# Performance work log

Measured on AMD Instinct MI355X. Metric: run time of the kernel, lower is better.

Reference implementation:

```python
import jax, jax.numpy as jnp
import numpy as np

NV, NF, DIM = 6144, 12288, 256


def _linear(x, W, b):
    # torch nn.Linear: x @ W.T + b, W has shape (out, in)
    return x @ W.T + b


def _agg(X, A, Wf, bf, Wg, bg):
    # AGG: out_fc = Linear(A @ X); out_gagg = Linear(A @ out_fc)  (eval mode: dropout is identity)
    out_fc = _linear(A @ X, Wf, bf)
    out_g = _linear(A @ out_fc, Wg, bg)
    return jax.nn.relu(out_fc + out_g)


def setup_inputs() -> dict:
    key = jax.random.key(0)
    ks = jax.random.split(key, 18)
    primal = jax.random.normal(ks[0], (NV, DIM), jnp.float32)
    # degree-normalized adjacency (docstring): scale uniform entries by 1/N for stable row sums
    A_primal = jax.random.uniform(ks[1], (NV, NV), jnp.float32) * (1.0 / NV)
    A_dual = jax.random.uniform(ks[2], (NF, NF), jnp.float32) * (1.0 / NF)
    A = jax.random.uniform(ks[3], (NV, NF), jnp.float32) * (1.0 / NF)
    faces = jax.random.randint(ks[4], (NF, 3), 0, NV)

    w = lambda k, shp: jax.random.normal(k, shp, jnp.float32) * 0.05
    return {
        "primal": primal, "A_primal": A_primal, "A_dual": A_dual, "A": A, "faces": faces,
        # 3 primal AGG layers (fc + gagg), stacked on leading axis
        "pW": w(ks[5], (3, DIM, DIM)), "pb": w(ks[6], (3, DIM)),
        "pgW": w(ks[7], (3, DIM, DIM)), "pgb": w(ks[8], (3, DIM)),
        # 3 dual AGG layers
        "dW": w(ks[9], (3, DIM, DIM)), "db": w(ks[10], (3, DIM)),
        "dgW": w(ks[11], (3, DIM, DIM)), "dgb": w(ks[12], (3, DIM)),
        # PDF linears: (dim, 2*dim)
        "Wp": w(ks[13], (DIM, 2 * DIM)), "bp": w(ks[14], (DIM,)),
        "Wd": w(ks[15], (DIM, 2 * DIM)), "bd": w(ks[16], (DIM,)),
    }


def reference(primal, A_primal, A_dual, A, faces, pW, pb, pgW, pgb, dW, db, dgW, dgb, Wp, bp, Wd, bd):
    x_p = primal
    x_d = (1.0 / 3.0) * (A.T @ primal)  # primal_dual
    primal_outs, dual_outs = [], []
    for i in range(3):
        primal_outs.append(x_p)
        x_p = _agg(x_p, A_primal, pW[i], pb[i], pgW[i], pgb[i]) + x_p
    for i in range(3):
        dual_outs.append(x_d)
        x_d = _agg(x_d, A_dual, dW[i], db[i], dgW[i], dgb[i]) + x_d
    # PDF: DAP gather-reduce  (N_f, 3, dim) -> (N_f, dim)
    f = jnp.mean(jnp.abs(x_p[faces] - x_d[:, None, :]), axis=1)
    out_dual = jax.nn.relu(_linear(jnp.concatenate([x_d, f], axis=1), Wd, bd))
    mapped = A @ f  # dual_primal
    out_primal = jax.nn.relu(_linear(jnp.concatenate([x_p, mapped], axis=1), Wp, bp))
    return (out_primal + x_p, out_dual + x_d, *primal_outs, *dual_outs)
```

## Files before the change

### kernel.cpp

```cpp
#include <hip/hip_runtime.h>


typedef short short8 __attribute__((ext_vector_type(8)));
typedef float floatx4 __attribute__((ext_vector_type(4)));
typedef unsigned short u16;

#define DIMN 256
#define GBM 128
#define GBN 256
#define GBK 64

static const int kNV = 6144;
static const int kNF = 12288;
static const int SLAB = 768;

__device__ __forceinline__ float bf2f(u16 u) {
  union { unsigned int i; float f; } x; x.i = ((unsigned int)u) << 16; return x.f;
}
__device__ __forceinline__ u16 f2bf(float f) {
  union { float f; unsigned int i; } x; x.f = f;
  unsigned int r = x.i + 0x7fffu + ((x.i >> 16) & 1u);
  return (u16)(r >> 16);
}
__device__ __forceinline__ void gld_lds16(const void* g, void* l) {
  __builtin_amdgcn_global_load_lds((__attribute__((address_space(1))) void*)(g),
                                   (__attribute__((address_space(3))) void*)(l),
                                   16, 0, 0);
}

__global__ __launch_bounds__(512, 1)
void gemm_bf16_k(const void* __restrict__ A0, int A0is32,
                 const void* __restrict__ A1, int A1is32, int K1,
                 int lda0, int lda1,
                 const void* __restrict__ Bt, int Btis32, int ldb,
                 float* __restrict__ P, int M, int kchunk)
{
  __shared__ __align__(16) u16 As[2][GBM * GBK];
  __shared__ __align__(16) u16 Bs[2][GBN * GBK];

  const int m0 = blockIdx.x * GBM;
  const int kb = blockIdx.z * kchunk;
  const int nkt = kchunk / GBK;

  const int tid = threadIdx.x;
  const int wid = tid >> 6;
  const int lane = tid & 63;
  const int wr = wid >> 2;
  const int wc = wid & 3;
  const int srow = lane >> 3;
  const int skk = (lane & 7) << 3;

  floatx4 acc[4][4];
  floatx4 zz = {0.f, 0.f, 0.f, 0.f};
#pragma unroll
  for (int i = 0; i < 4; ++i)
#pragma unroll
    for (int j = 0; j < 4; ++j) acc[i][j] = zz;

  auto stage = [&](int buf, int k0) {
    const void* base; int lda, is32, kl;
    if (k0 < K1) { base = A0; lda = lda0; is32 = A0is32; kl = k0; }
    else         { base = A1; lda = lda1; is32 = A1is32; kl = k0 - K1; }
    if (is32) {
      const float* F = (const float*)base;
#pragma unroll
      for (int j = 0; j < 2; ++j) {
        int c = (wid << 1) + j;
        const float* src = F + (size_t)(m0 + (c << 3) + srow) * lda + kl + skk;
        floatx4 f0 = *(const floatx4*)src;
        floatx4 f1 = *(const floatx4*)(src + 4);
        short8 v;
#pragma unroll
        for (int e = 0; e < 4; ++e) { v[e] = (short)f2bf(f0[e]); v[4 + e] = (short)f2bf(f1[e]); }
        *(short8*)&As[buf][(c << 9) + (lane << 3)] = v;
      }
    } else {
      const u16* U = (const u16*)base;
#pragma unroll
      for (int j = 0; j < 2; ++j) {
        int c = (wid << 1) + j;
        gld_lds16(U + (size_t)(m0 + (c << 3) + srow) * lda + kl + skk,
                  (void*)&As[buf][c << 9]);
      }
    }
    if (Btis32) {
      const float* F = (const float*)Bt;
#pragma unroll
      for (int j = 0; j < 4; ++j) {
        int c = (wid << 2) + j;
        const float* src = F + (size_t)((c << 3) + srow) * ldb + k0 + skk;
        floatx4 f0 = *(const floatx4*)src;
        floatx4 f1 = *(const floatx4*)(src + 4);
        short8 v;
#pragma unroll
        for (int e = 0; e < 4; ++e) { v[e] = (short)f2bf(f0[e]); v[4 + e] = (short)f2bf(f1[e]); }
        *(short8*)&Bs[buf][(c << 9) + (lane << 3)] = v;
      }
    } else {
      const u16* U = (const u16*)Bt;
#pragma unroll
      for (int j = 0; j < 4; ++j) {
        int c = (wid << 2) + j;
        gld_lds16(U + (size_t)((c << 3) + srow) * ldb + k0 + skk,
                  (void*)&Bs[buf][c << 9]);
      }
    }
  };

  int cur = 0;
  stage(0, kb);
  for (int kt = 0; kt < nkt; ++kt) {
    __syncthreads();
    if (kt + 1 < nkt) stage(cur ^ 1, kb + (kt + 1) * GBK);
#pragma unroll
    for (int ks = 0; ks < 2; ++ks) {
      short8 a[4], b[4];
      const int ko = (ks << 5) + ((lane >> 4) << 3);
#pragma unroll
      for (int mi = 0; mi < 4; ++mi)
        a[mi] = *(const short8*)&As[cur][((wr << 6) + (mi << 4) + (lane & 15)) * GBK + ko];
#pragma unroll
      for (int ni = 0; ni < 4; ++ni)
        b[ni] = *(const short8*)&Bs[cur][((wc << 6) + (ni << 4) + (lane & 15)) * GBK + ko];
#pragma unroll
      for (int mi = 0; mi < 4; ++mi)
#pragma unroll
        for (int ni = 0; ni < 4; ++ni)
          acc[mi][ni] = __builtin_amdgcn_mfma_f32_16x16x32_bf16(a[mi], b[ni], acc[mi][ni], 0, 0, 0);
    }
    cur ^= 1;
  }

  float* Pz = P + (size_t)blockIdx.z * (size_t)M * DIMN;
#pragma unroll
  for (int mi = 0; mi < 4; ++mi) {
#pragma unroll
    for (int ni = 0; ni < 4; ++ni) {
      const int mb = m0 + (wr << 6) + (mi << 4) + ((lane >> 4) << 2);
      const int n = (wc << 6) + (ni << 4) + (lane & 15);
#pragma unroll
      for (int r = 0; r < 4; ++r)
        Pz[(size_t)(mb + r) * DIMN + n] = acc[mi][ni][r];
    }
  }
}

__global__ __launch_bounds__(256)
void finalize_k(const float* __restrict__ P, int S, int Mrows, float scale,
                const float* __restrict__ bias, const u16* __restrict__ addmat,
                int do_relu, const float* __restrict__ resid,
                float* __restrict__ out, u16* __restrict__ out16)
{
  const size_t MN = (size_t)Mrows * DIMN;
  const size_t i4 = (((size_t)blockIdx.x * blockDim.x) + threadIdx.x) * 4;
  if (i4 >= MN) return;
  floatx4 v = {0.f, 0.f, 0.f, 0.f};
  for (int s = 0; s < S; ++s) v += *(const floatx4*)(P + (size_t)s * MN + i4);
  const int n = (int)(i4 & 255);
  floatx4 bf = {0.f,0.f,0.f,0.f}, af = {0.f,0.f,0.f,0.f}, rf = {0.f,0.f,0.f,0.f};
  if (bias) bf = *(const floatx4*)(bias + n);
  if (addmat) {
#pragma unroll
    for (int j = 0; j < 4; ++j) af[j] = bf2f(addmat[i4 + j]);
  }
  if (resid) rf = *(const floatx4*)(resid + i4);
  floatx4 o;
#pragma unroll
  for (int j = 0; j < 4; ++j) {
    float t = v[j] * scale + bf[j] + af[j];
    if (do_relu) t = fmaxf(t, 0.f);
    o[j] = t + rf[j];
  }
  if (out) *(floatx4*)(out + i4) = o;
  if (out16) {
    unsigned long long q = 0;
#pragma unroll
    for (int j = 0; j < 4; ++j) q |= ((unsigned long long)f2bf(o[j])) << (16 * j);
    *(unsigned long long*)(out16 + i4) = q;
  }
}

__global__ __launch_bounds__(256)
void transpose_k(const void* __restrict__ in, int is32, int ldin,
                 u16* __restrict__ out, int ldout)
{
  __shared__ __align__(16) u16 t[64][64];
  const int c0 = blockIdx.x << 6;
  const int r0 = blockIdx.y << 6;
  const int tid = threadIdx.x;
  const int lr = tid >> 3;
  const int lc = (tid & 7) << 3;
#pragma unroll
  for (int h = 0; h < 2; ++h) {
    const int r = lr + (h << 5);
    short8 v;
    if (is32) {
      const float* F = (const float*)in;
      const float* src = F + (size_t)(r0 + r) * ldin + (c0 + lc);
      floatx4 f0 = *(const floatx4*)src;
      floatx4 f1 = *(const floatx4*)(src + 4);
#pragma unroll
      for (int e = 0; e < 4; ++e) { v[e] = (short)f2bf(f0[e]); v[4 + e] = (short)f2bf(f1[e]); }
    } else {
      v = *(const short8*)((const u16*)in + (size_t)(r0 + r) * ldin + (c0 + lc));
    }
    *(short8*)&t[r][lc ^ ((r >> 3) << 3)] = v;
  }
  __syncthreads();
#pragma unroll
  for (int h = 0; h < 2; ++h) {
    const int oc = lr + (h << 5);
    short8 v;
#pragma unroll
    for (int e = 0; e < 8; ++e)
      v[e] = (short)t[lc + e][oc ^ ((lc >> 3) << 3)];
    *(short8*)&out[(size_t)(c0 + oc) * ldout + (r0 + lc)] = v;
  }
}

__global__ __launch_bounds__(256)
void cvt8_k(const float* __restrict__ in, u16* __restrict__ out, size_t n)
{
  const size_t i = (((size_t)blockIdx.x << 8) + threadIdx.x) << 3;
  if (i >= n) return;
  floatx4 f0 = *(const floatx4*)(in + i);
  floatx4 f1 = *(const floatx4*)(in + i + 4);
  short8 v;
#pragma unroll
  for (int e = 0; e < 4; ++e) { v[e] = (short)f2bf(f0[e]); v[4 + e] = (short)f2bf(f1[e]); }
  *(short8*)(out + i) = v;
}

__global__ __launch_bounds__(256)
void face_gather_k(const float* __restrict__ xp, const float* __restrict__ xd,
                   const int* __restrict__ faces, u16* __restrict__ f)
{
  const int fi = blockIdx.x;
  const int j = threadIdx.x;
  const int a = faces[fi * 3 + 0];
  const int b = faces[fi * 3 + 1];
  const int c = faces[fi * 3 + 2];
  const float xv = xd[(size_t)fi * DIMN + j];
  const float s = fabsf(xp[(size_t)a * DIMN + j] - xv)
                + fabsf(xp[(size_t)b * DIMN + j] - xv)
                + fabsf(xp[(size_t)c * DIMN + j] - xv);
  f[(size_t)fi * DIMN + j] = f2bf(s * (1.0f / 3.0f));
}

extern "C" void kernel_launch(void* const* d_in, const int* in_sizes, int n_in,
                              void* d_out, int out_size, void* d_ws, size_t ws_size,
                              hipStream_t stream)
{
  (void)in_sizes; (void)n_in; (void)out_size;
  const float* primal   = (const float*)d_in[0];
  const float* A_primal = (const float*)d_in[1];
  const float* A_dual   = (const float*)d_in[2];
  const float* A        = (const float*)d_in[3];
  const int* faces      = (const int*)d_in[4];
  const float* pW  = (const float*)d_in[5];
  const float* pb  = (const float*)d_in[6];
  const float* pgW = (const float*)d_in[7];
  const float* pgb = (const float*)d_in[8];
  const float* dW  = (const float*)d_in[9];
  const float* db  = (const float*)d_in[10];
  const float* dgW = (const float*)d_in[11];
  const float* dgb = (const float*)d_in[12];
  const float* Wp  = (const float*)d_in[13];
  const float* bp  = (const float*)d_in[14];
  const float* Wd  = (const float*)d_in[15];
  const float* bd  = (const float*)d_in[16];

  char* wsp = (char*)d_ws;
  auto alloc = [&](size_t bytes) -> void* {
    void* p = (void*)wsp;
    wsp += (bytes + 255) & ~(size_t)255;
    return p;
  };
  const size_t NVD = (size_t)kNV * DIMN, NFD = (size_t)kNF * DIMN;
  u16* XT    = (u16*)alloc(NFD * 2);
  u16* TB    = (u16*)alloc((size_t)SLAB * kNV * 2);
  u16* t1    = (u16*)alloc(NFD * 2);
  u16* fc    = (u16*)alloc(NFD * 2);
  float* P   = (float*)alloc((size_t)8 * NFD * 4);
  const size_t bigElems = (size_t)kNF * kNF + (size_t)kNF * kNV +
                          (size_t)kNV * kNF + (size_t)kNV * kNV + 1048576;
  const size_t need = (size_t)(wsp - (char*)d_ws) + bigElems * 2 + 4096;
  const bool big = ws_size >= need;
  u16 *Ad16 = nullptr, *At16 = nullptr, *A16 = nullptr, *Ap16 = nullptr, *W16 = nullptr;
  if (big) {
    Ad16 = (u16*)alloc((size_t)kNF * kNF * 2);
    At16 = (u16*)alloc((size_t)kNF * kNV * 2);
    A16  = (u16*)alloc((size_t)kNV * kNF * 2);
    Ap16 = (u16*)alloc((size_t)kNV * kNV * 2);
    W16  = (u16*)alloc((size_t)1048576 * 2);
  }

  float* out0  = (float*)d_out;
  float* out1  = out0 + NVD;
  float* pouts = out1 + NFD;
  float* douts = pouts + 3 * NVD;

  auto gemm = [&](const void* A0p, int a0is32, int lda0,
                  const void* A1p, int a1is32, int lda1, int K1,
                  const void* Btp, int btis32, int ldb, int M, int K, int S) {
    gemm_bf16_k<<<dim3(M / GBM, 1, S), dim3(512), 0, stream>>>(
        A0p, a0is32, A1p, a1is32, K1, lda0, lda1, Btp, btis32, ldb, P, M, K / S);
  };
  auto fin = [&](int M, int S, float scale, const float* bias, const u16* add,
                 int relu, const float* resid, float* out, u16* out16) {
    finalize_k<<<dim3((unsigned)((size_t)M * DIMN / 1024)), dim3(256), 0, stream>>>(
        P, S, M, scale, bias, add, relu, resid, out, out16);
  };
  auto tranp = [&](const void* in, int is32, int ldin, u16* out, int ldout,
                   int R, int C) {
    transpose_k<<<dim3(C / 64, R / 64), dim3(256), 0, stream>>>(
        in, is32, ldin, out, ldout);
  };
  auto cvt = [&](const float* in, u16* out, size_t n) {
    cvt8_k<<<dim3((unsigned)(n / 2048)), dim3(256), 0, stream>>>(in, out, n);
  };

  const void *AdP, *ApP, *AP, *pWP, *pgWP, *dWP, *dgWP, *WpP, *WdP;
  int cf;
  if (big) {
    cvt(A_dual, Ad16, (size_t)kNF * kNF);
    cvt(A_primal, Ap16, (size_t)kNV * kNV);
    cvt(A, A16, (size_t)kNV * kNF);
    tranp(A, 1, kNF, At16, kNV, kNV, kNF);
    cvt(pW,  W16 + 0,      196608);
    cvt(pgW, W16 + 196608, 196608);
    cvt(dW,  W16 + 393216, 196608);
    cvt(dgW, W16 + 589824, 196608);
    cvt(Wp,  W16 + 786432, 131072);
    cvt(Wd,  W16 + 917504, 131072);
    AdP = Ad16; ApP = Ap16; AP = A16; cf = 0;
    pWP = W16; pgWP = W16 + 196608; dWP = W16 + 393216; dgWP = W16 + 589824;
    WpP = W16 + 786432; WdP = W16 + 917504;
  } else {
    AdP = A_dual; ApP = A_primal; AP = A; cf = 1;
    pWP = pW; pgWP = pgW; dWP = dW; dgWP = dgW; WpP = Wp; WdP = Wd;
  }
  const size_t W3 = 65536;

  tranp(primal, 1, DIMN, XT, kNV, kNV, DIMN);
  hipMemcpyAsync(pouts, primal, NVD * 4, hipMemcpyDeviceToDevice, stream);

  if (big) {
    gemm(At16, 0, kNV, nullptr, 0, 0, kNV, XT, 0, kNV, kNF, kNV, 8);
    fin(kNF, 8, 1.0f / 3.0f, nullptr, nullptr, 0, nullptr, douts, nullptr);
  } else {
    for (int s = 0; s < kNF / SLAB; ++s) {
      const int m0 = s * SLAB;
      tranp(A + m0, 1, kNF, TB, kNV, kNV, SLAB);
      gemm(TB, 0, kNV, nullptr, 0, 0, kNV, XT, 0, kNV, SLAB, kNV, 16);
      fin(SLAB, 16, 1.0f / 3.0f, nullptr, nullptr, 0, nullptr,
          douts + (size_t)m0 * DIMN, nullptr);
    }
  }

  const float* xpc = primal;
  for (int i = 0; i < 3; ++i) {
    gemm(ApP, cf, kNV, nullptr, 0, 0, kNV, XT, 0, kNV, kNV, kNV, 16);
    fin(kNV, 16, 1.f, nullptr, nullptr, 0, nullptr, nullptr, t1);
    gemm(t1, 0, 256, nullptr, 0, 0, 256, (const u16*)pWP + i * W3, cf, 256,
         kNV, 256, 4);
    fin(kNV, 4, 1.f, pb + i * 256, nullptr, 0, nullptr, nullptr, fc);
    tranp(fc, 0, DIMN, TB, kNV, kNV, DIMN);
    gemm(ApP, cf, kNV, nullptr, 0, 0, kNV, TB, 0, kNV, kNV, kNV, 16);
    fin(kNV, 16, 1.f, nullptr, nullptr, 0, nullptr, nullptr, t1);
    gemm(t1, 0, 256, nullptr, 0, 0, 256, (const u16*)pgWP + i * W3, cf, 256,
         kNV, 256, 4);
    float* nxt = (i < 2) ? (pouts + (size_t)(i + 1) * NVD) : out0;
    fin(kNV, 4, 1.f, pgb + i * 256, fc, 1, xpc, nxt, nullptr);
    xpc = nxt;
    if (i < 2) tranp(xpc, 1, DIMN, XT, kNV, kNV, DIMN);
  }

  const float* xdc = douts;
  tranp(xdc, 1, DIMN, XT, kNF, kNF, DIMN);
  for (int i = 0; i < 3; ++i) {
    gemm(AdP, cf, kNF, nullptr, 0, 0, kNF, XT, 0, kNF, kNF, kNF, 8);
    fin(kNF, 8, 1.f, nullptr, nullptr, 0, nullptr, nullptr, t1);
    gemm(t1, 0, 256, nullptr, 0, 0, 256, (const u16*)dWP + i * W3, cf, 256,
         kNF, 256, 4);
    fin(kNF, 4, 1.f, db + i * 256, nullptr, 0, nullptr, nullptr, fc);
    tranp(fc, 0, DIMN, TB, kNF, kNF, DIMN);
    gemm(AdP, cf, kNF, nullptr, 0, 0, kNF, TB, 0, kNF, kNF, kNF, 8);
    fin(kNF, 8, 1.f, nullptr, nullptr, 0, nullptr, nullptr, t1);
    gemm(t1, 0, 256, nullptr, 0, 0, 256, (const u16*)dgWP + i * W3, cf, 256,
         kNF, 256, 4);
    float* nxt = (i < 2) ? (douts + (size_t)(i + 1) * NFD) : out1;
    fin(kNF, 4, 1.f, dgb + i * 256, fc, 1, xdc, nxt, nullptr);
    xdc = nxt;
    if (i < 2) tranp(xdc, 1, DIMN, XT, kNF, kNF, DIMN);
  }

  face_gather_k<<<dim3(kNF), dim3(256), 0, stream>>>(xpc, xdc, faces, t1);
  tranp(t1, 0, DIMN, TB, kNF, kNF, DIMN);
  gemm(xdc, 1, 256, t1, 0, 256, 256, WdP, cf, 512, kNF, 512, 8);
  fin(kNF, 8, 1.f, bd, nullptr, 1, xdc, out1, nullptr);
  gemm(AP, cf, kNF, nullptr, 0, 0, kNF, TB, 0, kNF, kNV, kNF, 16);
  fin(kNV, 16, 1.f, nullptr, nullptr, 0, nullptr, nullptr, fc);
  gemm(xpc, 1, 256, fc, 0, 256, 256, WpP, cf, 512, kNV, 512, 8);
  fin(kNV, 8, 1.f, bp, nullptr, 1, xpc, out0, nullptr);
}
```

Before: 2.162 ms.

## Fuse linear epilogues into GEMM, store split-K partials as bf16, drop conversions

The small 256-wide linear GEMMs now run without split-K and apply bias, add, relu and residual directly in the GEMM epilogue. This removes their separate finalize launches and the fp32 partial round trip. The big adjacency GEMMs write split-K partials in bf16 instead of fp32, halving partial-buffer traffic at some cost in precision. The weight and A bf16 conversion passes are also dropped: weights and A are read as fp32 and converted inside the GEMM, trading the upfront cvt work for in-kernel conversion and a single-block-per-row grid on the linear GEMMs.

```diff
diff --git a/kernel.cpp b/kernel.cpp
--- a/kernel.cpp
+++ b/kernel.cpp
@@ -3,6 +3,7 @@
 
 typedef short short8 __attribute__((ext_vector_type(8)));
 typedef float floatx4 __attribute__((ext_vector_type(4)));
+typedef unsigned short ushort4v __attribute__((ext_vector_type(4)));
 typedef unsigned short u16;
 
 #define DIMN 256
@@ -33,7 +34,11 @@
                  const void* __restrict__ A1, int A1is32, int K1,
                  int lda0, int lda1,
                  const void* __restrict__ Bt, int Btis32, int ldb,
-                 float* __restrict__ P, int M, int kchunk)
+                 void* __restrict__ P, int M, int kchunk, int pbf16,
+                 int fused, const float* __restrict__ bias,
+                 const u16* __restrict__ addmat, int do_relu,
+                 const float* __restrict__ resid,
+                 float* __restrict__ outf, u16* __restrict__ out16)
 {
   __shared__ __align__(16) u16 As[2][GBM * GBK];
   __shared__ __align__(16) u16 Bs[2][GBN * GBK];
@@ -131,22 +136,57 @@
     cur ^= 1;
   }
 
-  float* Pz = P + (size_t)blockIdx.z * (size_t)M * DIMN;
-#pragma unroll
-  for (int mi = 0; mi < 4; ++mi) {
-#pragma unroll
-    for (int ni = 0; ni < 4; ++ni) {
-      const int mb = m0 + (wr << 6) + (mi << 4) + ((lane >> 4) << 2);
-      const int n = (wc << 6) + (ni << 4) + (lane & 15);
-#pragma unroll
-      for (int r = 0; r < 4; ++r)
-        Pz[(size_t)(mb + r) * DIMN + n] = acc[mi][ni][r];
+  if (fused) {
+#pragma unroll
+    for (int mi = 0; mi < 4; ++mi) {
+#pragma unroll
+      for (int ni = 0; ni < 4; ++ni) {
+        const int mb = m0 + (wr << 6) + (mi << 4) + ((lane >> 4) << 2);
+        const int n = (wc << 6) + (ni << 4) + (lane & 15);
+        const float bv = bias ? bias[n] : 0.f;
+#pragma unroll
+        for (int r = 0; r < 4; ++r) {
+          const size_t idx = (size_t)(mb + r) * DIMN + n;
+          float t = acc[mi][ni][r] + bv;
+          if (addmat) t += bf2f(addmat[idx]);
+          if (do_relu) t = fmaxf(t, 0.f);
+          if (resid) t += resid[idx];
+          if (outf) outf[idx] = t;
+          if (out16) out16[idx] = f2bf(t);
+        }
+      }
+    }
+  } else if (pbf16) {
+    u16* Pz = (u16*)P + (size_t)blockIdx.z * (size_t)M * DIMN;
+#pragma unroll
+    for (int mi = 0; mi < 4; ++mi) {
+#pragma unroll
+      for (int ni = 0; ni < 4; ++ni) {
+        const int mb = m0 + (wr << 6) + (mi << 4) + ((lane >> 4) << 2);
+        const int n = (wc << 6) + (ni << 4) + (lane & 15);
+#pragma unroll
+        for (int r = 0; r < 4; ++r)
+          Pz[(size_t)(mb + r) * DIMN + n] = f2bf(acc[mi][ni][r]);
+      }
+    }
+  } else {
+    float* Pz = (float*)P + (size_t)blockIdx.z * (size_t)M * DIMN;
+#pragma unroll
+    for (int mi = 0; mi < 4; ++mi) {
+#pragma unroll
+      for (int ni = 0; ni < 4; ++ni) {
+        const int mb = m0 + (wr << 6) + (mi << 4) + ((lane >> 4) << 2);
+        const int n = (wc << 6) + (ni << 4) + (lane & 15);
+#pragma unroll
+        for (int r = 0; r < 4; ++r)
+          Pz[(size_t)(mb + r) * DIMN + n] = acc[mi][ni][r];
+      }
     }
   }
 }
 
 __global__ __launch_bounds__(256)
-void finalize_k(const float* __restrict__ P, int S, int Mrows, float scale,
+void finalize_k(const void* __restrict__ P, int pbf16, int S, int Mrows, float scale,
                 const float* __restrict__ bias, const u16* __restrict__ addmat,
                 int do_relu, const float* __restrict__ resid,
                 float* __restrict__ out, u16* __restrict__ out16)
@@ -155,7 +195,17 @@
   const size_t i4 = (((size_t)blockIdx.x * blockDim.x) + threadIdx.x) * 4;
   if (i4 >= MN) return;
   floatx4 v = {0.f, 0.f, 0.f, 0.f};
-  for (int s = 0; s < S; ++s) v += *(const floatx4*)(P + (size_t)s * MN + i4);
+  if (pbf16) {
+    const u16* Pu = (const u16*)P;
+    for (int s = 0; s < S; ++s) {
+      ushort4v p4 = *(const ushort4v*)(Pu + (size_t)s * MN + i4);
+#pragma unroll
+      for (int j = 0; j < 4; ++j) v[j] += bf2f(p4[j]);
+    }
+  } else {
+    const float* Pf = (const float*)P;
+    for (int s = 0; s < S; ++s) v += *(const floatx4*)(Pf + (size_t)s * MN + i4);
+  }
   const int n = (int)(i4 & 255);
   floatx4 bf = {0.f,0.f,0.f,0.f}, af = {0.f,0.f,0.f,0.f}, rf = {0.f,0.f,0.f,0.f};
   if (bias) bf = *(const floatx4*)(bias + n);
@@ -281,18 +331,15 @@
   u16* TB    = (u16*)alloc((size_t)SLAB * kNV * 2);
   u16* t1    = (u16*)alloc(NFD * 2);
   u16* fc    = (u16*)alloc(NFD * 2);
-  float* P   = (float*)alloc((size_t)8 * NFD * 4);
-  const size_t bigElems = (size_t)kNF * kNF + (size_t)kNF * kNV +
-                          (size_t)kNV * kNF + (size_t)kNV * kNV + 1048576;
+  void* P    = alloc((size_t)8 * NFD * 4);
+  const size_t bigElems = (size_t)kNF * kNF + (size_t)kNF * kNV + (size_t)kNV * kNV;
   const size_t need = (size_t)(wsp - (char*)d_ws) + bigElems * 2 + 4096;
   const bool big = ws_size >= need;
-  u16 *Ad16 = nullptr, *At16 = nullptr, *A16 = nullptr, *Ap16 = nullptr, *W16 = nullptr;
+  u16 *Ad16 = nullptr, *At16 = nullptr, *Ap16 = nullptr;
   if (big) {
     Ad16 = (u16*)alloc((size_t)kNF * kNF * 2);
     At16 = (u16*)alloc((size_t)kNF * kNV * 2);
-    A16  = (u16*)alloc((size_t)kNV * kNF * 2);
     Ap16 = (u16*)alloc((size_t)kNV * kNV * 2);
-    W16  = (u16*)alloc((size_t)1048576 * 2);
   }
 
   float* out0  = (float*)d_out;
@@ -300,16 +347,24 @@
   float* pouts = out1 + NFD;
   float* douts = pouts + 3 * NVD;
 
-  auto gemm = [&](const void* A0p, int a0is32, int lda0,
-                  const void* A1p, int a1is32, int lda1, int K1,
-                  const void* Btp, int btis32, int ldb, int M, int K, int S) {
+  auto gemmP = [&](const void* A0p, int a0is32, int lda0,
+                   const void* Btp, int ldb, int M, int K, int S) {
     gemm_bf16_k<<<dim3(M / GBM, 1, S), dim3(512), 0, stream>>>(
-        A0p, a0is32, A1p, a1is32, K1, lda0, lda1, Btp, btis32, ldb, P, M, K / S);
-  };
-  auto fin = [&](int M, int S, float scale, const float* bias, const u16* add,
-                 int relu, const float* resid, float* out, u16* out16) {
+        A0p, a0is32, nullptr, 0, K, lda0, 0, Btp, 0, ldb, P, M, K / S, 1,
+        0, nullptr, nullptr, 0, nullptr, nullptr, nullptr);
+  };
+  auto gemmF = [&](const void* A0p, int a0is32, int lda0,
+                   const void* A1p, int a1is32, int lda1, int K1,
+                   const float* Btp, int ldb, int M, int K,
+                   const float* bias, const u16* add, int relu,
+                   const float* resid, float* outf, u16* out16) {
+    gemm_bf16_k<<<dim3(M / GBM, 1, 1), dim3(512), 0, stream>>>(
+        A0p, a0is32, A1p, a1is32, K1, lda0, lda1, Btp, 1, ldb, P, M, K, 0,
+        1, bias, add, relu, resid, outf, out16);
+  };
+  auto fin = [&](int M, int S, float scale, float* out, u16* out16) {
     finalize_k<<<dim3((unsigned)((size_t)M * DIMN / 1024)), dim3(256), 0, stream>>>(
-        P, S, M, scale, bias, add, relu, resid, out, out16);
+        P, 1, S, M, scale, nullptr, nullptr, 0, nullptr, out, out16);
   };
   auto tranp = [&](const void* in, int is32, int ldin, u16* out, int ldout,
                    int R, int C) {
@@ -320,58 +375,44 @@
     cvt8_k<<<dim3((unsigned)(n / 2048)), dim3(256), 0, stream>>>(in, out, n);
   };
 
-  const void *AdP, *ApP, *AP, *pWP, *pgWP, *dWP, *dgWP, *WpP, *WdP;
+  const void *AdP, *ApP;
   int cf;
   if (big) {
     cvt(A_dual, Ad16, (size_t)kNF * kNF);
     cvt(A_primal, Ap16, (size_t)kNV * kNV);
-    cvt(A, A16, (size_t)kNV * kNF);
     tranp(A, 1, kNF, At16, kNV, kNV, kNF);
-    cvt(pW,  W16 + 0,      196608);
-    cvt(pgW, W16 + 196608, 196608);
-    cvt(dW,  W16 + 393216, 196608);
-    cvt(dgW, W16 + 589824, 196608);
-    cvt(Wp,  W16 + 786432, 131072);
-    cvt(Wd,  W16 + 917504, 131072);
-    AdP = Ad16; ApP = Ap16; AP = A16; cf = 0;
-    pWP = W16; pgWP = W16 + 196608; dWP = W16 + 393216; dgWP = W16 + 589824;
-    WpP = W16 + 786432; WdP = W16 + 917504;
+    AdP = Ad16; ApP = Ap16; cf = 0;
   } else {
-    AdP = A_dual; ApP = A_primal; AP = A; cf = 1;
-    pWP = pW; pgWP = pgW; dWP = dW; dgWP = dgW; WpP = Wp; WdP = Wd;
-  }
-  const size_t W3 = 65536;
+    AdP = A_dual; ApP = A_primal; cf = 1;
+  }
 
   tranp(primal, 1, DIMN, XT, kNV, kNV, DIMN);
   hipMemcpyAsync(pouts, primal, NVD * 4, hipMemcpyDeviceToDevice, stream);
 
   if (big) {
-    gemm(At16, 0, kNV, nullptr, 0, 0, kNV, XT, 0, kNV, kNF, kNV, 8);
-    fin(kNF, 8, 1.0f / 3.0f, nullptr, nullptr, 0, nullptr, douts, nullptr);
+    gemmP(At16, 0, kNV, XT, kNV, kNF, kNV, 8);
+    fin(kNF, 8, 1.0f / 3.0f, douts, nullptr);
   } else {
     for (int s = 0; s < kNF / SLAB; ++s) {
       const int m0 = s * SLAB;
       tranp(A + m0, 1, kNF, TB, kNV, kNV, SLAB);
-      gemm(TB, 0, kNV, nullptr, 0, 0, kNV, XT, 0, kNV, SLAB, kNV, 16);
-      fin(SLAB, 16, 1.0f / 3.0f, nullptr, nullptr, 0, nullptr,
-          douts + (size_t)m0 * DIMN, nullptr);
+      gemmP(TB, 0, kNV, XT, kNV, SLAB, kNV, 16);
+      fin(SLAB, 16, 1.0f / 3.0f, douts + (size_t)m0 * DIMN, nullptr);
     }
   }
 
   const float* xpc = primal;
   for (int i = 0; i < 3; ++i) {
-    gemm(ApP, cf, kNV, nullptr, 0, 0, kNV, XT, 0, kNV, kNV, kNV, 16);
-    fin(kNV, 16, 1.f, nullptr, nullptr, 0, nullptr, nullptr, t1);
-    gemm(t1, 0, 256, nullptr, 0, 0, 256, (const u16*)pWP + i * W3, cf, 256,
-         kNV, 256, 4);
-    fin(kNV, 4, 1.f, pb + i * 256, nullptr, 0, nullptr, nullptr, fc);
+    gemmP(ApP, cf, kNV, XT, kNV, kNV, kNV, 16);
+    fin(kNV, 16, 1.f, nullptr, t1);
+    gemmF(t1, 0, 256, nullptr, 0, 0, 256, pW + (size_t)i * 65536, 256,
+          kNV, 256, pb + i * 256, nullptr, 0, nullptr, nullptr, fc);
     tranp(fc, 0, DIMN, TB, kNV, kNV, DIMN);
-    gemm(ApP, cf, kNV, nullptr, 0, 0, kNV, TB, 0, kNV, kNV, kNV, 16);
-    fin(kNV, 16, 1.f, nullptr, nullptr, 0, nullptr, nullptr, t1);
-    gemm(t1, 0, 256, nullptr, 0, 0, 256, (const u16*)pgWP + i * W3, cf, 256,
-         kNV, 256, 4);
+    gemmP(ApP, cf, kNV, TB, kNV, kNV, kNV, 16);
+    fin(kNV, 16, 1.f, nullptr, t1);
     float* nxt = (i < 2) ? (pouts + (size_t)(i + 1) * NVD) : out0;
-    fin(kNV, 4, 1.f, pgb + i * 256, fc, 1, xpc, nxt, nullptr);
+    gemmF(t1, 0, 256, nullptr, 0, 0, 256, pgW + (size_t)i * 65536, 256,
+          kNV, 256, pgb + i * 256, fc, 1, xpc, nxt, nullptr);
     xpc = nxt;
     if (i < 2) tranp(xpc, 1, DIMN, XT, kNV, kNV, DIMN);
   }
@@ -379,28 +420,26 @@
   const float* xdc = douts;
   tranp(xdc, 1, DIMN, XT, kNF, kNF, DIMN);
   for (int i = 0; i < 3; ++i) {
-    gemm(AdP, cf, kNF, nullptr, 0, 0, kNF, XT, 0, kNF, kNF, kNF, 8);
-    fin(kNF, 8, 1.f, nullptr, nullptr, 0, nullptr, nullptr, t1);
-    gemm(t1, 0, 256, nullptr, 0, 0, 256, (const u16*)dWP + i * W3, cf, 256,
-         kNF, 256, 4);
-    fin(kNF, 4, 1.f, db + i * 256, nullptr, 0, nullptr, nullptr, fc);
+    gemmP(AdP, cf, kNF, XT, kNF, kNF, kNF, 8);
+    fin(kNF, 8, 1.f, nullptr, t1);
+    gemmF(t1, 0, 256, nullptr, 0, 0, 256, dW + (size_t)i * 65536, 256,
+          kNF, 256, db + i * 256, nullptr, 0, nullptr, nullptr, fc);
     tranp(fc, 0, DIMN, TB, kNF, kNF, DIMN);
-    gemm(AdP, cf, kNF, nullptr, 0, 0, kNF, TB, 0, kNF, kNF, kNF, 8);
-    fin(kNF, 8, 1.f, nullptr, nullptr, 0, nullptr, nullptr, t1);
-    gemm(t1, 0, 256, nullptr, 0, 0, 256, (const u16*)dgWP + i * W3, cf, 256,
-         kNF, 256, 4);
+    gemmP(AdP, cf, kNF, TB, kNF, kNF, kNF, 8);
+    fin(kNF, 8, 1.f, nullptr, t1);
     float* nxt = (i < 2) ? (douts + (size_t)(i + 1) * NFD) : out1;
-    fin(kNF, 4, 1.f, dgb + i * 256, fc, 1, xdc, nxt, nullptr);
+    gemmF(t1, 0, 256, nullptr, 0, 0, 256, dgW + (size_t)i * 65536, 256,
+          kNF, 256, dgb + i * 256, fc, 1, xdc, nxt, nullptr);
     xdc = nxt;
     if (i < 2) tranp(xdc, 1, DIMN, XT, kNF, kNF, DIMN);
   }
 
   face_gather_k<<<dim3(kNF), dim3(256), 0, stream>>>(xpc, xdc, faces, t1);
   tranp(t1, 0, DIMN, TB, kNF, kNF, DIMN);
-  gemm(xdc, 1, 256, t1, 0, 256, 256, WdP, cf, 512, kNF, 512, 8);
-  fin(kNF, 8, 1.f, bd, nullptr, 1, xdc, out1, nullptr);
-  gemm(AP, cf, kNF, nullptr, 0, 0, kNF, TB, 0, kNF, kNV, kNF, 16);
-  fin(kNV, 16, 1.f, nullptr, nullptr, 0, nullptr, nullptr, fc);
-  gemm(xpc, 1, 256, fc, 0, 256, 256, WpP, cf, 512, kNV, 512, 8);
-  fin(kNV, 8, 1.f, bp, nullptr, 1, xpc, out0, nullptr);
-}
+  gemmF(xdc, 1, 256, t1, 0, 256, 256, Wd, 512, kNF, 512,
+        bd, nullptr, 1, xdc, out1, nullptr);
+  gemmP(A, 1, kNF, TB, kNF, kNV, kNF, 16);
+  fin(kNV, 16, 1.f, nullptr, fc);
+  gemmF(xpc, 1, 256, fc, 0, 256, 256, Wp, 512, kNV, 512,
+        bp, nullptr, 1, xpc, out0, nullptr);
+}
```

After: 2.128 ms. No clear change (-1.6%).
